# Performance work log

Hardware: AMD Instinct MI355X
Metric: run time of the kernel (lower is better)

## Reference

```python
import jax, jax.numpy as jnp
import numpy as np

TEMPERATURE = 2.0
RAD2DEG = 180.0 / np.pi


def _safe_norm(diff, axis=-1):
    # L2 norm with zero (sub)gradient at 0, matching torch's convention and
    # avoiding NaNs on the (later-discarded) diagonal of pairwise distances.
    d2 = jnp.sum(diff * diff, axis=axis)
    pos = d2 > 0
    return jnp.where(pos, jnp.sqrt(jnp.where(pos, d2, 1.0)), 0.0)


def _rot6d_to_matrix(d6):
    # pytorch3d.transforms.rotation_6d_to_matrix: Gram-Schmidt on two 3-vectors.
    a1, a2 = d6[..., :3], d6[..., 3:6]
    b1 = a1 / jnp.linalg.norm(a1, axis=-1, keepdims=True)
    a2p = a2 - jnp.sum(b1 * a2, axis=-1, keepdims=True) * b1
    b2 = a2p / jnp.linalg.norm(a2p, axis=-1, keepdims=True)
    b3 = jnp.cross(b1, b2)
    return jnp.stack([b1, b2, b3], axis=-2)  # [n, 3, 3], rows b1,b2,b3


def _pose_error(pose):
    rot = _rot6d_to_matrix(pose[:, :6])                    # [n,3,3]
    div = jnp.power(jnp.linalg.det(rot), 1.0 / 3.0)[:, None, None]
    rot = rot / div
    t = pose[:, 6:]                                        # [n,3]
    # trace(rot_i @ rot_j^T) = sum_ab rot_i[a,b]*rot_j[a,b]
    r_trace = jnp.einsum('iab,jab->ij', rot, rot)          # [n,n]
    cos_theta = (r_trace - 1.0) / 2.0
    theta = jnp.arccos(jnp.clip(cos_theta, -1.0, 1.0)) * RAD2DEG
    shift = _safe_norm(t[:, None, :] - t[None, :, :]) * 100.0
    return theta, shift


def reference(features, labels):
    n = features.shape[0]
    theta_diffs, shift_diffs = _pose_error(labels)

    # FeatureSimilarity('l2'): -||f_i - f_j|| / t
    logits = -_safe_norm(features[:, None, :] - features[None, :, :]) / TEMPERATURE
    logits = logits - jax.lax.stop_gradient(jnp.max(logits, axis=1, keepdims=True))
    exp_logits = jnp.exp(logits)

    # Drop diagonal -> [n, n-1], preserving ascending column order (masked_select).
    cols = jnp.arange(n - 1)
    jidx = cols[None, :] + (cols[None, :] >= jnp.arange(n)[:, None]).astype(cols.dtype)
    take = lambda x: jnp.take_along_axis(x, jidx, axis=1)
    L = take(logits)          # [n, n-1]
    E = take(exp_logits)      # [n, n-1]
    TD = take(theta_diffs)    # [n, n-1]
    SD = take(shift_diffs)    # [n, n-1]

    # Vectorize the k-loop: M[i,k,j] = diffs[i,j] >= diffs[i,k]
    mt = TD[:, None, :] >= TD[:, :, None]                 # [n, n-1, n-1]
    ms = SD[:, None, :] >= SD[:, :, None]
    denom_t = jnp.sum(jnp.where(mt, E[:, None, :], 0.0), axis=-1)  # [n, n-1]
    denom_s = jnp.sum(jnp.where(ms, E[:, None, :], 0.0), axis=-1)

    pos_log_probs = (2.0 * L - jnp.log(denom_t) - jnp.log(denom_s)) / 2.0
    return -jnp.sum(pos_log_probs) / (n * (n - 1))


def setup_inputs() -> dict:
    key = jax.random.key(0)
    k1, k2 = jax.random.split(key)
    features = jax.random.normal(k1, (512, 256), dtype=jnp.float32)
    labels = jax.random.normal(k2, (512, 9), dtype=jnp.float32)
    return {"features": features, "labels": labels}
```

## Files before the change

### kernel.cpp

```cpp
#include <hip/hip_runtime.h>
#include <math.h>

#define N 512
#define D 256
#define ITILE 2
#define TPB 512
#define NPAIRS 261632.0f

__constant__ float kRad2Deg = 57.29577951308232f;

__global__ void prep_kernel(const float* __restrict__ labels,
                            float* __restrict__ rot,
                            float* __restrict__ tvec,
                            float* __restrict__ acc) {
    int i = blockIdx.x * blockDim.x + threadIdx.x;
    if (i == 0) acc[0] = 0.0f;
    if (i >= N) return;
    const float* p = labels + i * 9;
    float a1x = p[0], a1y = p[1], a1z = p[2];
    float a2x = p[3], a2y = p[4], a2z = p[5];
    float n1 = sqrtf(a1x * a1x + a1y * a1y + a1z * a1z);
    float b1x = a1x / n1, b1y = a1y / n1, b1z = a1z / n1;
    float dp = b1x * a2x + b1y * a2y + b1z * a2z;
    float cx = a2x - dp * b1x, cy = a2y - dp * b1y, cz = a2z - dp * b1z;
    float n2 = sqrtf(cx * cx + cy * cy + cz * cz);
    float b2x = cx / n2, b2y = cy / n2, b2z = cz / n2;
    float b3x = b1y * b2z - b1z * b2y;
    float b3y = b1z * b2x - b1x * b2z;
    float b3z = b1x * b2y - b1y * b2x;
    float det = b1x * (b2y * b3z - b2z * b3y)
              - b1y * (b2x * b3z - b2z * b3x)
              + b1z * (b2x * b3y - b2y * b3x);
    float inv = 1.0f / cbrtf(det);
    float* r = rot + i * 9;
    r[0] = b1x * inv; r[1] = b1y * inv; r[2] = b1z * inv;
    r[3] = b2x * inv; r[4] = b2y * inv; r[5] = b2z * inv;
    r[6] = b3x * inv; r[7] = b3y * inv; r[8] = b3z * inv;
    tvec[i * 3 + 0] = p[6];
    tvec[i * 3 + 1] = p[7];
    tvec[i * 3 + 2] = p[8];
}

__global__ __launch_bounds__(TPB) void rowdata_kernel(
        const float* __restrict__ f,
        const float* __restrict__ rot,
        const float* __restrict__ tvec,
        float* __restrict__ E,
        float* __restrict__ TD,
        float* __restrict__ SD,
        float* __restrict__ acc) {
    __shared__ __attribute__((aligned(16))) float lds_fi[ITILE * D];
    __shared__ float red[TPB / 64];

    const int j  = threadIdx.x;
    const int i0 = blockIdx.x * ITILE;

    lds_fi[j] = f[i0 * D + j];
    __syncthreads();

    float d2[ITILE];
#pragma unroll
    for (int r = 0; r < ITILE; ++r) d2[r] = 0.0f;

    const float4* __restrict__ fj4 = (const float4*)(f + j * D);
#pragma unroll
    for (int kk = 0; kk < D / 4; ++kk) {
        float4 v = fj4[kk];
#pragma unroll
        for (int r = 0; r < ITILE; ++r) {
            const float4 fi = *(const float4*)&lds_fi[r * D + kk * 4];
            float dx = fi.x - v.x, dy = fi.y - v.y;
            float dz = fi.z - v.z, dw = fi.w - v.w;
            d2[r] += dx * dx + dy * dy + dz * dz + dw * dw;
        }
    }

    float rj[9];
#pragma unroll
    for (int c = 0; c < 9; ++c) rj[c] = rot[j * 9 + c];
    const float tjx = tvec[j * 3 + 0];
    const float tjy = tvec[j * 3 + 1];
    const float tjz = tvec[j * 3 + 2];

    float lsum = 0.0f;
#pragma unroll
    for (int r = 0; r < ITILE; ++r) {
        const int i = i0 + r;
        float tr = 0.0f;
#pragma unroll
        for (int c = 0; c < 9; ++c) tr += rot[i * 9 + c] * rj[c];
        float ct = (tr - 1.0f) * 0.5f;
        ct = fminf(1.0f, fmaxf(-1.0f, ct));
        float theta = acosf(ct) * kRad2Deg;

        float dx = tvec[i * 3 + 0] - tjx;
        float dy = tvec[i * 3 + 1] - tjy;
        float dz = tvec[i * 3 + 2] - tjz;
        float sd2 = dx * dx + dy * dy + dz * dz;
        float shift = (sd2 > 0.0f ? sqrtf(sd2) : 0.0f) * 100.0f;

        float dist = (d2[r] > 0.0f ? sqrtf(d2[r]) : 0.0f);
        float L = -dist * 0.5f;
        float Ev = (j == i) ? 0.0f : expf(L);
        E[i * N + j]  = Ev;
        TD[i * N + j] = theta;
        SD[i * N + j] = shift;
        lsum += L;
    }

#pragma unroll
    for (int off = 32; off > 0; off >>= 1) lsum += __shfl_down(lsum, off, 64);
    const int lane = j & 63, wid = j >> 6;
    if (lane == 0) red[wid] = lsum;
    __syncthreads();
    if (j == 0) {
        float s = 0.0f;
#pragma unroll
        for (int w = 0; w < TPB / 64; ++w) s += red[w];
        atomicAdd(acc, s);
    }
}

__global__ __launch_bounds__(256) void sortdenom_kernel(
        const float* __restrict__ E,
        const float* __restrict__ TD,
        const float* __restrict__ SD,
        float* __restrict__ acc) {
    __shared__ unsigned kT[512], kS[512];
    __shared__ float pT[512], pS[512];
    __shared__ float sT[512], sS[512];
    __shared__ int   lT[512], lS[512];
    __shared__ float redA[4], redB[4];
    __shared__ float diag_part_sh;

    const int t = threadIdx.x;
    const int i = blockIdx.x;
    const float* __restrict__ er = E  + i * N;
    const float* __restrict__ tr = TD + i * N;
    const float* __restrict__ sr = SD + i * N;

    const float e0 = er[t], e1 = er[t + 256];
    const float t0 = tr[t], t1 = tr[t + 256];
    const float s0 = sr[t], s1 = sr[t + 256];
    const float dT = tr[i], dS = sr[i];

    float dtd = ((t0 >= dT) ? e0 : 0.0f) + ((t1 >= dT) ? e1 : 0.0f);
    float dsd = ((s0 >= dS) ? e0 : 0.0f) + ((s1 >= dS) ? e1 : 0.0f);
#pragma unroll
    for (int off = 32; off > 0; off >>= 1) {
        dtd += __shfl_down(dtd, off, 64);
        dsd += __shfl_down(dsd, off, 64);
    }
    const int lane = t & 63, wid = t >> 6;
    if (lane == 0) { redA[wid] = dtd; redB[wid] = dsd; }

    kT[t] = __float_as_uint(t0); kT[t + 256] = __float_as_uint(t1);
    kS[t] = __float_as_uint(s0); kS[t + 256] = __float_as_uint(s1);
    pT[t] = e0; pT[t + 256] = e1;
    pS[t] = e0; pS[t + 256] = e1;
    __syncthreads();

    if (t == 0) {
        float a = redA[0] + redA[1] + redA[2] + redA[3];
        float b = redB[0] + redB[1] + redB[2] + redB[3];
        diag_part_sh = 0.5f * (logf(a) + logf(b));
    }

    for (unsigned k = 2; k <= 512; k <<= 1) {
        for (unsigned jj = k >> 1; jj >= 1; jj >>= 1) {
            __syncthreads();
            const unsigned a = ((t & ~(jj - 1)) << 1) | (t & (jj - 1));
            const unsigned b = a | jj;
            const bool up = ((a & k) == 0);
            {
                unsigned ka = kT[a], kb = kT[b];
                bool sw = up ? (ka > kb) : (ka < kb);
                if (sw) {
                    kT[a] = kb; kT[b] = ka;
                    float tp = pT[a]; pT[a] = pT[b]; pT[b] = tp;
                }
            }
            {
                unsigned ka = kS[a], kb = kS[b];
                bool sw = up ? (ka > kb) : (ka < kb);
                if (sw) {
                    kS[a] = kb; kS[b] = ka;
                    float tp = pS[a]; pS[a] = pS[b]; pS[b] = tp;
                }
            }
        }
    }
    __syncthreads();

    sT[t] = pT[t]; sT[t + 256] = pT[t + 256];
    sS[t] = pS[t]; sS[t + 256] = pS[t + 256];
    lT[t]       = (t == 0 || kT[t - 1]   != kT[t])       ? t         : 0;
    lT[t + 256] = (kT[t + 255] != kT[t + 256])           ? (t + 256) : 0;
    lS[t]       = (t == 0 || kS[t - 1]   != kS[t])       ? t         : 0;
    lS[t + 256] = (kS[t + 255] != kS[t + 256])           ? (t + 256) : 0;
    __syncthreads();

    for (int st = 1; st < 512; st <<= 1) {
        float a0 = (t + st < 512) ? sT[t + st] : 0.0f;
        float a1 = (t + 256 + st < 512) ? sT[t + 256 + st] : 0.0f;
        float b0 = (t + st < 512) ? sS[t + st] : 0.0f;
        float b1 = (t + 256 + st < 512) ? sS[t + 256 + st] : 0.0f;
        int   m0 = (t >= st) ? lT[t - st] : 0;
        int   m1 = lT[t + 256 - st];
        int   n0 = (t >= st) ? lS[t - st] : 0;
        int   n1 = lS[t + 256 - st];
        __syncthreads();
        sT[t] += a0; sT[t + 256] += a1;
        sS[t] += b0; sS[t + 256] += b1;
        lT[t] = max(lT[t], m0); lT[t + 256] = max(lT[t + 256], m1);
        lS[t] = max(lS[t], n0); lS[t + 256] = max(lS[t + 256], n1);
        __syncthreads();
    }

    float term = logf(sT[lT[t]]) + logf(sT[lT[t + 256]])
               + logf(sS[lS[t]]) + logf(sS[lS[t + 256]]);
#pragma unroll
    for (int off = 32; off > 0; off >>= 1) term += __shfl_down(term, off, 64);
    __syncthreads();
    if (lane == 0) redA[wid] = term;
    __syncthreads();
    if (t == 0) {
        float tt = redA[0] + redA[1] + redA[2] + redA[3];
        atomicAdd(acc, -0.5f * tt + diag_part_sh);
    }
}

__global__ void finalize_kernel(const float* __restrict__ acc,
                                float* __restrict__ out) {
    out[0] = -acc[0] / NPAIRS;
}

extern "C" void kernel_launch(void* const* d_in, const int* in_sizes, int n_in,
                              void* d_out, int out_size, void* d_ws, size_t ws_size,
                              hipStream_t stream) {
    const float* f      = (const float*)d_in[0];
    const float* labels = (const float*)d_in[1];
    float* out = (float*)d_out;
    float* ws  = (float*)d_ws;

    float* rot  = ws;
    float* tvec = rot + N * 9;
    float* acc  = tvec + N * 3;
    float* E    = acc + 4;
    float* TD   = E + N * N;
    float* SD   = TD + N * N;

    prep_kernel<<<2, 256, 0, stream>>>(labels, rot, tvec, acc);
    rowdata_kernel<<<N / ITILE, TPB, 0, stream>>>(f, rot, tvec, E, TD, SD, acc);
    sortdenom_kernel<<<N, 256, 0, stream>>>(E, TD, SD, acc);
    finalize_kernel<<<1, 1, 0, stream>>>(acc, out);
}
```

Baseline: 57.27 us.

## Use norm expansion for feature distances and pack sort key/payload into u64

Feature distances are computed as ||fi||^2+||fj||^2-2 fi·fj, with row norms precomputed in a widened prep kernel, reducing arithmetic in the distance loop. The bitonic sort now keeps key and exp payload in a single 64-bit word with a swizzled LDS index, halving LDS accesses per compare-swap and reducing bank conflicts. The expansion risks cancellation error for near-identical rows.

```diff
diff --git a/kernel.cpp b/kernel.cpp
--- a/kernel.cpp
+++ b/kernel.cpp
@@ -4,53 +4,68 @@
 #define N 512
 #define D 256
 #define ITILE 2
-#define TPB 512
 #define NPAIRS 261632.0f
 
+typedef unsigned long long u64;
+#define SW(x) ((x) ^ (((x) >> 4) & 15))
+
 __constant__ float kRad2Deg = 57.29577951308232f;
 
-__global__ void prep_kernel(const float* __restrict__ labels,
-                            float* __restrict__ rot,
-                            float* __restrict__ tvec,
-                            float* __restrict__ acc) {
-    int i = blockIdx.x * blockDim.x + threadIdx.x;
-    if (i == 0) acc[0] = 0.0f;
-    if (i >= N) return;
-    const float* p = labels + i * 9;
-    float a1x = p[0], a1y = p[1], a1z = p[2];
-    float a2x = p[3], a2y = p[4], a2z = p[5];
-    float n1 = sqrtf(a1x * a1x + a1y * a1y + a1z * a1z);
-    float b1x = a1x / n1, b1y = a1y / n1, b1z = a1z / n1;
-    float dp = b1x * a2x + b1y * a2y + b1z * a2z;
-    float cx = a2x - dp * b1x, cy = a2y - dp * b1y, cz = a2z - dp * b1z;
-    float n2 = sqrtf(cx * cx + cy * cy + cz * cz);
-    float b2x = cx / n2, b2y = cy / n2, b2z = cz / n2;
-    float b3x = b1y * b2z - b1z * b2y;
-    float b3y = b1z * b2x - b1x * b2z;
-    float b3z = b1x * b2y - b1y * b2x;
-    float det = b1x * (b2y * b3z - b2z * b3y)
-              - b1y * (b2x * b3z - b2z * b3x)
-              + b1z * (b2x * b3y - b2y * b3x);
-    float inv = 1.0f / cbrtf(det);
-    float* r = rot + i * 9;
-    r[0] = b1x * inv; r[1] = b1y * inv; r[2] = b1z * inv;
-    r[3] = b2x * inv; r[4] = b2y * inv; r[5] = b2z * inv;
-    r[6] = b3x * inv; r[7] = b3y * inv; r[8] = b3z * inv;
-    tvec[i * 3 + 0] = p[6];
-    tvec[i * 3 + 1] = p[7];
-    tvec[i * 3 + 2] = p[8];
-}
-
-__global__ __launch_bounds__(TPB) void rowdata_kernel(
+__global__ __launch_bounds__(64) void prep_kernel(
+        const float* __restrict__ f,
+        const float* __restrict__ labels,
+        float* __restrict__ rot,
+        float* __restrict__ tvec,
+        float* __restrict__ nrm,
+        float* __restrict__ acc) {
+    const int i = blockIdx.x;
+    const int l = threadIdx.x;
+
+    const float4 v = ((const float4*)(f + i * D))[l];
+    float ss = v.x * v.x + v.y * v.y + v.z * v.z + v.w * v.w;
+#pragma unroll
+    for (int off = 32; off > 0; off >>= 1) ss += __shfl_down(ss, off, 64);
+
+    if (l == 0) {
+        nrm[i] = ss;
+        const float* p = labels + i * 9;
+        float a1x = p[0], a1y = p[1], a1z = p[2];
+        float a2x = p[3], a2y = p[4], a2z = p[5];
+        float n1 = sqrtf(a1x * a1x + a1y * a1y + a1z * a1z);
+        float b1x = a1x / n1, b1y = a1y / n1, b1z = a1z / n1;
+        float dp = b1x * a2x + b1y * a2y + b1z * a2z;
+        float cx = a2x - dp * b1x, cy = a2y - dp * b1y, cz = a2z - dp * b1z;
+        float n2 = sqrtf(cx * cx + cy * cy + cz * cz);
+        float b2x = cx / n2, b2y = cy / n2, b2z = cz / n2;
+        float b3x = b1y * b2z - b1z * b2y;
+        float b3y = b1z * b2x - b1x * b2z;
+        float b3z = b1x * b2y - b1y * b2x;
+        float det = b1x * (b2y * b3z - b2z * b3y)
+                  - b1y * (b2x * b3z - b2z * b3x)
+                  + b1z * (b2x * b3y - b2y * b3x);
+        float inv = 1.0f / cbrtf(det);
+        float* r = rot + i * 9;
+        r[0] = b1x * inv; r[1] = b1y * inv; r[2] = b1z * inv;
+        r[3] = b2x * inv; r[4] = b2y * inv; r[5] = b2z * inv;
+        r[6] = b3x * inv; r[7] = b3y * inv; r[8] = b3z * inv;
+        tvec[i * 3 + 0] = p[6];
+        tvec[i * 3 + 1] = p[7];
+        tvec[i * 3 + 2] = p[8];
+        if (i == 0) acc[0] = 0.0f;
+    }
+}
+
+__global__ __launch_bounds__(512) void rowdata_kernel(
         const float* __restrict__ f,
         const float* __restrict__ rot,
         const float* __restrict__ tvec,
+        const float* __restrict__ nrm,
         float* __restrict__ E,
         float* __restrict__ TD,
         float* __restrict__ SD,
         float* __restrict__ acc) {
     __shared__ __attribute__((aligned(16))) float lds_fi[ITILE * D];
-    __shared__ float red[TPB / 64];
+    __shared__ float red[8];
 
     const int j  = threadIdx.x;
     const int i0 = blockIdx.x * ITILE;
@@ -58,22 +73,18 @@
     lds_fi[j] = f[i0 * D + j];
     __syncthreads();
 
-    float d2[ITILE];
-#pragma unroll
-    for (int r = 0; r < ITILE; ++r) d2[r] = 0.0f;
-
+    float dot0 = 0.0f, dot1 = 0.0f;
     const float4* __restrict__ fj4 = (const float4*)(f + j * D);
-#pragma unroll
+#pragma unroll 16
     for (int kk = 0; kk < D / 4; ++kk) {
-        float4 v = fj4[kk];
-#pragma unroll
-        for (int r = 0; r < ITILE; ++r) {
-            const float4 fi = *(const float4*)&lds_fi[r * D + kk * 4];
-            float dx = fi.x - v.x, dy = fi.y - v.y;
-            float dz = fi.z - v.z, dw = fi.w - v.w;
-            d2[r] += dx * dx + dy * dy + dz * dz + dw * dw;
-        }
-    }
+        const float4 v = fj4[kk];
+        const float4 a = *(const float4*)&lds_fi[kk * 4];
+        const float4 b = *(const float4*)&lds_fi[D + kk * 4];
+        dot0 += a.x * v.x; dot0 += a.y * v.y; dot0 += a.z * v.z; dot0 += a.w * v.w;
+        dot1 += b.x * v.x; dot1 += b.y * v.y; dot1 += b.z * v.z; dot1 += b.w * v.w;
+    }
+    const float nj  = nrm[j];
+    const float dotr[2] = { dot0, dot1 };
 
     float rj[9];
 #pragma unroll
@@ -99,9 +110,14 @@
         float sd2 = dx * dx + dy * dy + dz * dz;
         float shift = (sd2 > 0.0f ? sqrtf(sd2) : 0.0f) * 100.0f;
 
-        float dist = (d2[r] > 0.0f ? sqrtf(d2[r]) : 0.0f);
-        float L = -dist * 0.5f;
-        float Ev = (j == i) ? 0.0f : expf(L);
+        float d2 = nrm[i] + nj - 2.0f * dotr[r];
+        float L, Ev;
+        if (j == i) { L = 0.0f; Ev = 0.0f; }
+        else {
+            float dist = (d2 > 0.0f ? sqrtf(d2) : 0.0f);
+            L  = -dist * 0.5f;
+            Ev = expf(L);
+        }
         E[i * N + j]  = Ev;
         TD[i * N + j] = theta;
         SD[i * N + j] = shift;
@@ -116,7 +132,7 @@
     if (j == 0) {
         float s = 0.0f;
 #pragma unroll
-        for (int w = 0; w < TPB / 64; ++w) s += red[w];
+        for (int w = 0; w < 8; ++w) s += red[w];
         atomicAdd(acc, s);
     }
 }
@@ -126,8 +142,7 @@
         const float* __restrict__ TD,
         const float* __restrict__ SD,
         float* __restrict__ acc) {
-    __shared__ unsigned kT[512], kS[512];
-    __shared__ float pT[512], pS[512];
+    __shared__ u64   qT[512], qS[512];
     __shared__ float sT[512], sS[512];
     __shared__ int   lT[512], lS[512];
     __shared__ float redA[4], redB[4];
@@ -154,10 +169,10 @@
     const int lane = t & 63, wid = t >> 6;
     if (lane == 0) { redA[wid] = dtd; redB[wid] = dsd; }
 
-    kT[t] = __float_as_uint(t0); kT[t + 256] = __float_as_uint(t1);
-    kS[t] = __float_as_uint(s0); kS[t + 256] = __float_as_uint(s1);
-    pT[t] = e0; pT[t + 256] = e1;
-    pS[t] = e0; pS[t + 256] = e1;
+    qT[SW(t)]       = ((u64)__float_as_uint(t0) << 32) | (u64)__float_as_uint(e0);
+    qT[SW(t + 256)] = ((u64)__float_as_uint(t1) << 32) | (u64)__float_as_uint(e1);
+    qS[SW(t)]       = ((u64)__float_as_uint(s0) << 32) | (u64)__float_as_uint(e0);
+    qS[SW(t + 256)] = ((u64)__float_as_uint(s1) << 32) | (u64)__float_as_uint(e1);
     __syncthreads();
 
     if (t == 0) {
@@ -173,31 +188,35 @@
             const unsigned b = a | jj;
             const bool up = ((a & k) == 0);
             {
-                unsigned ka = kT[a], kb = kT[b];
-                bool sw = up ? (ka > kb) : (ka < kb);
-                if (sw) {
-                    kT[a] = kb; kT[b] = ka;
-                    float tp = pT[a]; pT[a] = pT[b]; pT[b] = tp;
-                }
+                u64 va = qT[SW(a)], vb = qT[SW(b)];
+                if (up ? (va > vb) : (va < vb)) { qT[SW(a)] = vb; qT[SW(b)] = va; }
             }
             {
-                unsigned ka = kS[a], kb = kS[b];
-                bool sw = up ? (ka > kb) : (ka < kb);
-                if (sw) {
-                    kS[a] = kb; kS[b] = ka;
-                    float tp = pS[a]; pS[a] = pS[b]; pS[b] = tp;
-                }
+                u64 va = qS[SW(a)], vb = qS[SW(b)];
+                if (up ? (va > vb) : (va < vb)) { qS[SW(a)] = vb; qS[SW(b)] = va; }
             }
         }
     }
     __syncthreads();
 
-    sT[t] = pT[t]; sT[t + 256] = pT[t + 256];
-    sS[t] = pS[t]; sS[t + 256] = pS[t + 256];
-    lT[t]       = (t == 0 || kT[t - 1]   != kT[t])       ? t         : 0;
-    lT[t + 256] = (kT[t + 255] != kT[t + 256])           ? (t + 256) : 0;
-    lS[t]       = (t == 0 || kS[t - 1]   != kS[t])       ? t         : 0;
-    lS[t + 256] = (kS[t + 255] != kS[t + 256])           ? (t + 256) : 0;
+    {
+        const u64 v0 = qT[SW(t)],       v1 = qT[SW(t + 256)];
+        sT[t]       = __uint_as_float((unsigned)v0);
+        sT[t + 256] = __uint_as_float((unsigned)v1);
+        const unsigned h0 = (unsigned)(v0 >> 32), h1 = (unsigned)(v1 >> 32);
+        const unsigned hp1 = (unsigned)(qT[SW(t + 255)] >> 32);
+        lT[t]       = (t == 0 || (unsigned)(qT[SW(t - 1)] >> 32) != h0) ? t : 0;
+        lT[t + 256] = (hp1 != h1) ? (t + 256) : 0;
+    }
+    {
+        const u64 v0 = qS[SW(t)],       v1 = qS[SW(t + 256)];
+        sS[t]       = __uint_as_float((unsigned)v0);
+        sS[t + 256] = __uint_as_float((unsigned)v1);
+        const unsigned h0 = (unsigned)(v0 >> 32), h1 = (unsigned)(v1 >> 32);
+        const unsigned hp1 = (unsigned)(qS[SW(t + 255)] >> 32);
+        lS[t]       = (t == 0 || (unsigned)(qS[SW(t - 1)] >> 32) != h0) ? t : 0;
+        lS[t + 256] = (hp1 != h1) ? (t + 256) : 0;
+    }
     __syncthreads();
 
     for (int st = 1; st < 512; st <<= 1) {
@@ -245,13 +264,14 @@
 
     float* rot  = ws;
     float* tvec = rot + N * 9;
-    float* acc  = tvec + N * 3;
+    float* nrm  = tvec + N * 3;
+    float* acc  = nrm + N;
     float* E    = acc + 4;
     float* TD   = E + N * N;
     float* SD   = TD + N * N;
 
-    prep_kernel<<<2, 256, 0, stream>>>(labels, rot, tvec, acc);
-    rowdata_kernel<<<N / ITILE, TPB, 0, stream>>>(f, rot, tvec, E, TD, SD, acc);
+    prep_kernel<<<N, 64, 0, stream>>>(f, labels, rot, tvec, nrm, acc);
+    rowdata_kernel<<<N / ITILE, 512, 0, stream>>>(f, rot, tvec, nrm, E, TD, SD, acc);
     sortdenom_kernel<<<N, 256, 0, stream>>>(E, TD, SD, acc);
     finalize_kernel<<<1, 1, 0, stream>>>(acc, out);
 }
```

Result: no change. 57.36 us (+0.2%).
